# Optimization experiments

Measured on AMD Instinct MI355X. Metric: run time of the kernel, lower is better.

Reference implementation:

```python
import jax, jax.numpy as jnp
import numpy as np

B, S, H, NH = 2, 2048, 1024, 16
HD = H // NH  # 64


def rope_cos_sin(seq_len, dim, base=10000.0, dtype=jnp.float32):
    inv_freq = 1.0 / (base ** (jnp.arange(0, dim, 2, dtype=jnp.float32) / dim))
    t = jnp.arange(seq_len, dtype=jnp.float32)
    freqs = jnp.outer(t, inv_freq)              # [S, dim/2]
    emb = jnp.concatenate([freqs, freqs], -1)   # [S, dim]
    # broadcast shape [1, S, 1, dim]
    return jnp.cos(emb)[None, :, None, :].astype(dtype), jnp.sin(emb)[None, :, None, :].astype(dtype)


def rotate_half(x):
    x1, x2 = x[..., : x.shape[-1] // 2], x[..., x.shape[-1] // 2:]
    return jnp.concatenate([-x2, x1], axis=-1)


def setup_inputs() -> dict:
    key = jax.random.key(0)
    ks = jax.random.split(key, 5)
    sc = 1.0 / np.sqrt(H)
    x = jax.random.normal(ks[0], (B, S, H), jnp.float32)
    Wq = jax.random.normal(ks[1], (H, H), jnp.float32) * sc
    Wk = jax.random.normal(ks[2], (H, H), jnp.float32) * sc
    Wv = jax.random.normal(ks[3], (H, H), jnp.float32) * sc
    Wo = jax.random.normal(ks[4], (H, H), jnp.float32) * sc
    z = jnp.zeros((H,), jnp.float32)
    mask = jnp.tril(jnp.ones((S, S), bool))[None, None]  # causal [1,1,S,S]
    return {"x": x, "Wq": Wq, "bq": z, "Wk": Wk, "bk": z, "Wv": Wv, "bv": z,
            "Wo": Wo, "bo": z, "mask": mask}


def reference(x, Wq, bq, Wk, bk, Wv, bv, Wo, bo, mask):
    b, s, _ = x.shape
    q = (x @ Wq.T + bq).reshape(b, s, NH, HD)
    k = (x @ Wk.T + bk).reshape(b, s, NH, HD)
    v = (x @ Wv.T + bv).reshape(b, s, NH, HD)
    cos, sin = rope_cos_sin(s, HD, dtype=x.dtype)
    q = q * cos + rotate_half(q) * sin
    k = k * cos + rotate_half(k) * sin
    # [b, h, s, s] scores, explicit as in original
    scores = jnp.einsum("bqhd,bkhd->bhqk", q, k) / jnp.sqrt(jnp.asarray(HD, x.dtype))
    scores = jnp.where(mask, scores, jnp.asarray(-jnp.inf, x.dtype))
    attn = jax.nn.softmax(scores, axis=-1)
    out = jnp.einsum("bhqk,bkhd->bqhd", attn, v).reshape(b, s, H)
    return out @ Wo.T + bo
```

## Files before the change

### kernel.cpp

```cpp
#include <hip/hip_runtime.h>

typedef __bf16 bf16;
typedef __bf16 bf16x4 __attribute__((ext_vector_type(4)));
typedef __bf16 bf16x8 __attribute__((ext_vector_type(8)));
typedef float floatx4 __attribute__((ext_vector_type(4)));

#define MFMA16(a, b, c) __builtin_amdgcn_mfma_f32_16x16x32_bf16(a, b, c, 0, 0, 0)

__device__ __forceinline__ void load_lds16(const void* g, void* l) {
    __builtin_amdgcn_global_load_lds(
        (const __attribute__((address_space(1))) unsigned int*)g,
        (__attribute__((address_space(3))) unsigned int*)l, 16, 0, 0);
}

__device__ __forceinline__ bf16x8 scale8(bf16x8 a, float s) {
    bf16x8 o;
    #pragma unroll
    for (int i = 0; i < 8; i++) o[i] = (bf16)((float)a[i] * s);
    return o;
}

#define WAITV4_BAR()  do { asm volatile("s_waitcnt vmcnt(4)" ::: "memory"); \
                           __builtin_amdgcn_s_barrier();                    \
                           __builtin_amdgcn_sched_barrier(0); } while (0)
#define WAITV2_BAR()  do { asm volatile("s_waitcnt vmcnt(2)" ::: "memory"); \
                           __builtin_amdgcn_s_barrier();                    \
                           __builtin_amdgcn_sched_barrier(0); } while (0)
#define WAITV0_BAR()  do { asm volatile("s_waitcnt vmcnt(0)" ::: "memory"); \
                           __builtin_amdgcn_s_barrier();                    \
                           __builtin_amdgcn_sched_barrier(0); } while (0)
#define TRAIL_BAR()   do { __builtin_amdgcn_sched_barrier(0);               \
                           asm volatile("s_waitcnt lgkmcnt(0)" ::: "memory"); \
                           __builtin_amdgcn_s_barrier(); } while (0)

__global__ __launch_bounds__(256) void cvt_all_kernel(
    const float* __restrict__ x, const float* __restrict__ wq,
    const float* __restrict__ wk, const float* __restrict__ wv,
    const float* __restrict__ wo,
    bf16* __restrict__ xb, bf16* __restrict__ wqb, bf16* __restrict__ wkb,
    bf16* __restrict__ wvb, bf16* __restrict__ wob)
{
    int bid = blockIdx.x;
    const float* src; bf16* dst; int off;
    if (bid < 4096)      { src = x;  dst = xb;  off = bid; }
    else if (bid < 5120) { src = wq; dst = wqb; off = bid - 4096; }
    else if (bid < 6144) { src = wk; dst = wkb; off = bid - 5120; }
    else if (bid < 7168) { src = wv; dst = wvb; off = bid - 6144; }
    else                 { src = wo; dst = wob; off = bid - 7168; }
    int idx = (off * 256 + threadIdx.x) * 4;
    float4 v = *(const float4*)&src[idx];
    bf16x4 o;
    o[0] = (bf16)v.x; o[1] = (bf16)v.y; o[2] = (bf16)v.z; o[3] = (bf16)v.w;
    *(bf16x4*)&dst[idx] = o;
}

__global__ __launch_bounds__(256) void cvt_kernel(const float* __restrict__ x,
                                                  bf16* __restrict__ xb) {
    int idx = (blockIdx.x * 256 + threadIdx.x) * 4;
    float4 v = *(const float4*)&x[idx];
    bf16x4 o;
    o[0] = (bf16)v.x; o[1] = (bf16)v.y; o[2] = (bf16)v.z; o[3] = (bf16)v.w;
    *(bf16x4*)&xb[idx] = o;
}


#define PREP_STAGE()                                                          \
    int u0 = w * 128 + lane;                                                  \
    int u1 = u0 + 64;                                                         \
    int r0_ = u0 >> 2, c0_ = ((u0 & 3) ^ ((r0_ >> 1) & 3)) * 8;               \
    int r1_ = u1 >> 2, c1_ = ((u1 & 3) ^ ((r1_ >> 1) & 3)) * 8;               \
    int du0 = w * 1024;                                                       \
    int du1 = du0 + 512;

#define STAGE_PF(Asrc, Bsrc, arow, brow, sbuf, kk0)                           \
    do {                                                                      \
        load_lds16(&Asrc[(size_t)((arow) + r0_) * 1024 + (kk0) + c0_],        \
                   &As[sbuf][0][0] + du0);                                    \
        load_lds16(&Asrc[(size_t)((arow) + r1_) * 1024 + (kk0) + c1_],        \
                   &As[sbuf][0][0] + du1);                                    \
        load_lds16(&Bsrc[(size_t)((brow) + r0_) * 1024 + (kk0) + c0_],        \
                   &Bs[sbuf][0][0] + du0);                                    \
        load_lds16(&Bsrc[(size_t)((brow) + r1_) * 1024 + (kk0) + c1_],        \
                   &Bs[sbuf][0][0] + du1);                                    \
    } while (0)

#define GEMM_CORE(Asrc, Bsrc, arow, brow)                                     \
    PREP_STAGE()                                                              \
    STAGE_PF(Asrc, Bsrc, arow, brow, 0, 0);                                   \
    _Pragma("unroll 2")                                                       \
    for (int s = 0; s < 32; s++) {                                            \
        int sb = s & 1;                                                       \
        if (s + 1 < 32) {                                                     \
            STAGE_PF(Asrc, Bsrc, arow, brow, sb ^ 1, (s + 1) * 32);           \
            WAITV4_BAR();                                                     \
        } else {                                                              \
            WAITV0_BAR();                                                     \
        }                                                                     \
        bf16x8 af[4], bfr[4];                                                 \
        _Pragma("unroll")                                                     \
        for (int mt = 0; mt < 4; mt++) {                                      \
            int row = wm + mt * 16 + l15;                                     \
            af[mt] = *(const bf16x8*)&As[sb][row][(quad ^ ((row >> 1) & 3)) * 8]; \
        }                                                                     \
        _Pragma("unroll")                                                     \
        for (int nt = 0; nt < 4; nt++) {                                      \
            int row = wn + nt * 16 + l15;                                     \
            bfr[nt] = *(const bf16x8*)&Bs[sb][row][(quad ^ ((row >> 1) & 3)) * 8]; \
        }                                                                     \
        __builtin_amdgcn_s_setprio(1);                                        \
        _Pragma("unroll")                                                     \
        for (int mt = 0; mt < 4; mt++)                                        \
            _Pragma("unroll")                                                 \
            for (int nt = 0; nt < 4; nt++)                                    \
                acc[mt][nt] = MFMA16(af[mt], bfr[nt], acc[mt][nt]);           \
        __builtin_amdgcn_s_setprio(0);                                        \
        TRAIL_BAR();                                                          \
    }

__global__ __launch_bounds__(256) void gemm_qkv_fast(
    const bf16* __restrict__ xb,
    const bf16* __restrict__ Wq, const bf16* __restrict__ Wk,
    const bf16* __restrict__ Wv,
    const float* __restrict__ bq, const float* __restrict__ bk,
    const float* __restrict__ bv,
    bf16* __restrict__ q_ws, bf16* __restrict__ k_ws, bf16* __restrict__ vt_ws)
{
    int m0 = blockIdx.x * 128;
    int n0 = blockIdx.y * 128;
    int sec = n0 >> 10;
    int nw0 = n0 & 1023;
    const bf16* W     = (sec == 0) ? Wq : (sec == 1) ? Wk : Wv;
    const float* bias = (sec == 0) ? bq : (sec == 1) ? bk : bv;

    __shared__ bf16 As[2][128][32];
    __shared__ bf16 Bs[2][128][32];

    int tid = threadIdx.x;
    int lane = tid & 63, w = tid >> 6;
    int l15 = lane & 15, quad = lane >> 4;
    int wm = (w >> 1) * 64, wn = (w & 1) * 64;

    floatx4 acc[4][4];
    #pragma unroll
    for (int i = 0; i < 4; i++)
        #pragma unroll
        for (int j = 0; j < 4; j++) acc[i][j] = (floatx4){0.f, 0.f, 0.f, 0.f};

    GEMM_CORE(xb, W, m0, nw0)

    if (sec < 2) {
        bf16* outp = (sec == 0) ? q_ws : k_ws;
        float inv[2];
        inv[0] = __expf(-(float)l15 * (9.210340371976184f / 32.0f));
        inv[1] = __expf(-(float)(16 + l15) * (9.210340371976184f / 32.0f));
        #pragma unroll
        for (int mt = 0; mt < 4; mt++) {
            #pragma unroll
            for (int r = 0; r < 4; r++) {
                int m = m0 + wm + mt * 16 + quad * 4 + r;
                int bb = m >> 11, s = m & 2047;
                #pragma unroll
                for (int nt = 0; nt < 2; nt++) {
                    int nl1 = nw0 + wn + nt * 16 + l15;
                    int nl2 = nl1 + 32;
                    float x1 = acc[mt][nt][r] + bias[nl1];
                    float x2 = acc[mt][nt + 2][r] + bias[nl2];
                    float ang = (float)s * inv[nt];
                    float sn, cs;
                    __sincosf(ang, &sn, &cs);
                    int hh = nl1 >> 6, d = nl1 & 63;
                    size_t base = ((size_t)(bb * 16 + hh) * 2048 + s) * 64;
                    outp[base + d]      = (bf16)(x1 * cs - x2 * sn);
                    outp[base + d + 32] = (bf16)(x2 * cs + x1 * sn);
                }
            }
        }
    } else {
        #pragma unroll
        for (int mt = 0; mt < 4; mt++) {
            int mbase = m0 + wm + mt * 16 + quad * 4;
            int bb = mbase >> 11, s0 = mbase & 2047;
            #pragma unroll
            for (int nt = 0; nt < 4; nt++) {
                int nl = nw0 + wn + nt * 16 + l15;
                int hh = nl >> 6, d = nl & 63;
                bf16x4 pk;
                #pragma unroll
                for (int r = 0; r < 4; r++) pk[r] = (bf16)(acc[mt][nt][r] + bias[nl]);
                *(bf16x4*)&vt_ws[((size_t)(bb * 16 + hh) * 64 + d) * 2048 + s0] = pk;
            }
        }
    }
}

__global__ __launch_bounds__(256) void gemm_out_fast(
    const bf16* __restrict__ A, const bf16* __restrict__ W,
    const float* __restrict__ bias, float* __restrict__ out)
{
    int m0 = blockIdx.x * 128;
    int n0 = blockIdx.y * 128;

    __shared__ bf16 As[2][128][32];
    __shared__ bf16 Bs[2][128][32];

    int tid = threadIdx.x;
    int lane = tid & 63, w = tid >> 6;
    int l15 = lane & 15, quad = lane >> 4;
    int wm = (w >> 1) * 64, wn = (w & 1) * 64;

    floatx4 acc[4][4];
    #pragma unroll
    for (int i = 0; i < 4; i++)
        #pragma unroll
        for (int j = 0; j < 4; j++) acc[i][j] = (floatx4){0.f, 0.f, 0.f, 0.f};

    GEMM_CORE(A, W, m0, n0)

    #pragma unroll
    for (int mt = 0; mt < 4; mt++) {
        #pragma unroll
        for (int r = 0; r < 4; r++) {
            int m = m0 + wm + mt * 16 + quad * 4 + r;
            #pragma unroll
            for (int nt = 0; nt < 4; nt++) {
                int nl = n0 + wn + nt * 16 + l15;
                out[(size_t)m * 1024 + nl] = acc[mt][nt][r] + bias[nl];
            }
        }
    }
}

__global__ __launch_bounds__(256) void gemm_qkv_f32w(
    const bf16* __restrict__ xb,
    const float* __restrict__ Wq, const float* __restrict__ Wk,
    const float* __restrict__ Wv,
    const float* __restrict__ bq, const float* __restrict__ bk,
    const float* __restrict__ bv,
    bf16* __restrict__ q_ws, bf16* __restrict__ k_ws, bf16* __restrict__ vt_ws)
{
    int m0 = blockIdx.x * 128;
    int n0 = blockIdx.y * 128;
    int sec = n0 >> 10;
    int nw0 = n0 & 1023;
    const float* W    = (sec == 0) ? Wq : (sec == 1) ? Wk : Wv;
    const float* bias = (sec == 0) ? bq : (sec == 1) ? bk : bv;

    __shared__ bf16 As[128][72];
    __shared__ bf16 Bs[128][72];

    int tid = threadIdx.x;
    int lane = tid & 63, w = tid >> 6;
    int l15 = lane & 15, quad = lane >> 4;
    int wm = (w >> 1) * 64, wn = (w & 1) * 64;
    int sr = tid >> 1;
    int sk = (tid & 1) * 32;

    floatx4 acc[4][4];
    #pragma unroll
    for (int i = 0; i < 4; i++)
        #pragma unroll
        for (int j = 0; j < 4; j++) acc[i][j] = (floatx4){0.f, 0.f, 0.f, 0.f};

    for (int k0 = 0; k0 < 1024; k0 += 64) {
        __syncthreads();
        const bf16* ap = &xb[(size_t)(m0 + sr) * 1024 + k0 + sk];
        bf16x8 a0 = *(const bf16x8*)(ap);
        bf16x8 a1 = *(const bf16x8*)(ap + 8);
        bf16x8 a2 = *(const bf16x8*)(ap + 16);
        bf16x8 a3 = *(const bf16x8*)(ap + 24);
        const float* wp = &W[(size_t)(nw0 + sr) * 1024 + k0 + sk];
        bf16x8 bv_[4];
        #pragma unroll
        for (int c = 0; c < 4; c++) {
            float4 f0 = *(const float4*)(wp + c * 8);
            float4 f1 = *(const float4*)(wp + c * 8 + 4);
            bf16x8 t;
            t[0] = (bf16)f0.x; t[1] = (bf16)f0.y; t[2] = (bf16)f0.z; t[3] = (bf16)f0.w;
            t[4] = (bf16)f1.x; t[5] = (bf16)f1.y; t[6] = (bf16)f1.z; t[7] = (bf16)f1.w;
            bv_[c] = t;
        }
        *(bf16x8*)&As[sr][sk + 0]  = a0;
        *(bf16x8*)&As[sr][sk + 8]  = a1;
        *(bf16x8*)&As[sr][sk + 16] = a2;
        *(bf16x8*)&As[sr][sk + 24] = a3;
        #pragma unroll
        for (int c = 0; c < 4; c++) *(bf16x8*)&Bs[sr][sk + c * 8] = bv_[c];
        __syncthreads();
        #pragma unroll
        for (int kk = 0; kk < 64; kk += 32) {
            bf16x8 af[4], bfr[4];
            #pragma unroll
            for (int mt = 0; mt < 4; mt++)
                af[mt] = *(const bf16x8*)&As[wm + mt * 16 + l15][kk + quad * 8];
            #pragma unroll
            for (int nt = 0; nt < 4; nt++)
                bfr[nt] = *(const bf16x8*)&Bs[wn + nt * 16 + l15][kk + quad * 8];
            #pragma unroll
            for (int mt = 0; mt < 4; mt++)
                #pragma unroll
                for (int nt = 0; nt < 4; nt++)
                    acc[mt][nt] = MFMA16(af[mt], bfr[nt], acc[mt][nt]);
        }
    }

    if (sec < 2) {
        bf16* outp = (sec == 0) ? q_ws : k_ws;
        float inv[2];
        inv[0] = __expf(-(float)l15 * (9.210340371976184f / 32.0f));
        inv[1] = __expf(-(float)(16 + l15) * (9.210340371976184f / 32.0f));
        #pragma unroll
        for (int mt = 0; mt < 4; mt++) {
            #pragma unroll
            for (int r = 0; r < 4; r++) {
                int m = m0 + wm + mt * 16 + quad * 4 + r;
                int bb = m >> 11, s = m & 2047;
                #pragma unroll
                for (int nt = 0; nt < 2; nt++) {
                    int nl1 = nw0 + wn + nt * 16 + l15;
                    int nl2 = nl1 + 32;
                    float x1 = acc[mt][nt][r] + bias[nl1];
                    float x2 = acc[mt][nt + 2][r] + bias[nl2];
                    float ang = (float)s * inv[nt];
                    float sn, cs;
                    __sincosf(ang, &sn, &cs);
                    int hh = nl1 >> 6, d = nl1 & 63;
                    size_t base = ((size_t)(bb * 16 + hh) * 2048 + s) * 64;
                    outp[base + d]      = (bf16)(x1 * cs - x2 * sn);
                    outp[base + d + 32] = (bf16)(x2 * cs + x1 * sn);
                }
            }
        }
    } else {
        #pragma unroll
        for (int mt = 0; mt < 4; mt++) {
            int mbase = m0 + wm + mt * 16 + quad * 4;
            int bb = mbase >> 11, s0 = mbase & 2047;
            #pragma unroll
            for (int nt = 0; nt < 4; nt++) {
                int nl = nw0 + wn + nt * 16 + l15;
                int hh = nl >> 6, d = nl & 63;
                bf16x4 pk;
                #pragma unroll
                for (int r = 0; r < 4; r++) pk[r] = (bf16)(acc[mt][nt][r] + bias[nl]);
                *(bf16x4*)&vt_ws[((size_t)(bb * 16 + hh) * 64 + d) * 2048 + s0] = pk;
            }
        }
    }
}

__global__ __launch_bounds__(256) void gemm_out_f32w(
    const bf16* __restrict__ A, const float* __restrict__ W,
    const float* __restrict__ bias, float* __restrict__ out)
{
    int m0 = blockIdx.x * 128;
    int n0 = blockIdx.y * 128;

    __shared__ bf16 As[128][72];
    __shared__ bf16 Bs[128][72];

    int tid = threadIdx.x;
    int lane = tid & 63, w = tid >> 6;
    int l15 = lane & 15, quad = lane >> 4;
    int wm = (w >> 1) * 64, wn = (w & 1) * 64;
    int sr = tid >> 1;
    int sk = (tid & 1) * 32;

    floatx4 acc[4][4];
    #pragma unroll
    for (int i = 0; i < 4; i++)
        #pragma unroll
        for (int j = 0; j < 4; j++) acc[i][j] = (floatx4){0.f, 0.f, 0.f, 0.f};

    for (int k0 = 0; k0 < 1024; k0 += 64) {
        __syncthreads();
        const bf16* ap = &A[(size_t)(m0 + sr) * 1024 + k0 + sk];
        bf16x8 a0 = *(const bf16x8*)(ap);
        bf16x8 a1 = *(const bf16x8*)(ap + 8);
        bf16x8 a2 = *(const bf16x8*)(ap + 16);
        bf16x8 a3 = *(const bf16x8*)(ap + 24);
        const float* wp = &W[(size_t)(n0 + sr) * 1024 + k0 + sk];
        bf16x8 bv_[4];
        #pragma unroll
        for (int c = 0; c < 4; c++) {
            float4 f0 = *(const float4*)(wp + c * 8);
            float4 f1 = *(const float4*)(wp + c * 8 + 4);
            bf16x8 t;
            t[0] = (bf16)f0.x; t[1] = (bf16)f0.y; t[2] = (bf16)f0.z; t[3] = (bf16)f0.w;
            t[4] = (bf16)f1.x; t[5] = (bf16)f1.y; t[6] = (bf16)f1.z; t[7] = (bf16)f1.w;
            bv_[c] = t;
        }
        *(bf16x8*)&As[sr][sk + 0]  = a0;
        *(bf16x8*)&As[sr][sk + 8]  = a1;
        *(bf16x8*)&As[sr][sk + 16] = a2;
        *(bf16x8*)&As[sr][sk + 24] = a3;
        #pragma unroll
        for (int c = 0; c < 4; c++) *(bf16x8*)&Bs[sr][sk + c * 8] = bv_[c];
        __syncthreads();
        #pragma unroll
        for (int kk = 0; kk < 64; kk += 32) {
            bf16x8 af[4], bfr[4];
            #pragma unroll
            for (int mt = 0; mt < 4; mt++)
                af[mt] = *(const bf16x8*)&As[wm + mt * 16 + l15][kk + quad * 8];
            #pragma unroll
            for (int nt = 0; nt < 4; nt++)
                bfr[nt] = *(const bf16x8*)&Bs[wn + nt * 16 + l15][kk + quad * 8];
            #pragma unroll
            for (int mt = 0; mt < 4; mt++)
                #pragma unroll
                for (int nt = 0; nt < 4; nt++)
                    acc[mt][nt] = MFMA16(af[mt], bfr[nt], acc[mt][nt]);
        }
    }

    #pragma unroll
    for (int mt = 0; mt < 4; mt++) {
        #pragma unroll
        for (int r = 0; r < 4; r++) {
            int m = m0 + wm + mt * 16 + quad * 4 + r;
            #pragma unroll
            for (int nt = 0; nt < 4; nt++) {
                int nl = n0 + wn + nt * 16 + l15;
                out[(size_t)m * 1024 + nl] = acc[mt][nt][r] + bias[nl];
            }
        }
    }
}

__global__ __launch_bounds__(512, 4) void attn_kernel(
    const bf16* __restrict__ q_ws, const bf16* __restrict__ k_ws,
    const bf16* __restrict__ vt_ws, bf16* __restrict__ o_ws)
{
    __shared__ bf16 Ks[2][64][64];
    __shared__ bf16 Vt[2][64][64];
    __shared__ bf16 Ps[8][16][72];

    int tid = threadIdx.x;
    int w = tid >> 6, lane = tid & 63;
    int l15 = lane & 15, quad = lane >> 4;

    int bid = blockIdx.x;
    int g = bid & 31;
    int xx = bid >> 5;
    int qt = (xx < 8) ? xx : 23 - xx;
    if (g & 1) qt = 15 - qt;
    int bb = g >> 4, h = g & 15;
    const bf16* qp = q_ws + (size_t)g * 2048 * 64;
    const bf16* kp = k_ws + (size_t)g * 2048 * 64;
    const bf16* vp = vt_ws + (size_t)g * 64 * 2048;
    int qrow = qt * 128 + w * 16;

    int r = w * 8 + (lane >> 3);
    int c = (lane & 7) ^ (r & 7);
    int od = w * 512;

    const float SCL = 0.125f * 1.4426950408889634f;
    const float MFIX = 20.0f;

    bf16x8 qf0 = scale8(*(const bf16x8*)&qp[(size_t)(qrow + l15) * 64 + quad * 8], SCL);
    bf16x8 qf1 = scale8(*(const bf16x8*)&qp[(size_t)(qrow + l15) * 64 + 32 + quad * 8], SCL);

    float l_lane = 0.f;
    floatx4 acc[4];
    #pragma unroll
    for (int nt = 0; nt < 4; nt++) acc[nt] = (floatx4){0.f, 0.f, 0.f, 0.f};

    int nkt = 2 * qt + 2;

    load_lds16(&kp[(size_t)r * 64 + c * 8], &Ks[0][0][0] + od);
    load_lds16(&vp[(size_t)r * 2048 + c * 8], &Vt[0][0][0] + od);

    for (int kt = 0; kt < nkt; kt++) {
        int buf = kt & 1;
        if (kt + 1 < nkt) {
            int kn0 = (kt + 1) * 64;
            load_lds16(&kp[(size_t)(kn0 + r) * 64 + c * 8], &Ks[buf ^ 1][0][0] + od);
            load_lds16(&vp[(size_t)r * 2048 + kn0 + c * 8], &Vt[buf ^ 1][0][0] + od);
            WAITV2_BAR();
        } else {
            WAITV0_BAR();
        }

        int kt0 = kt * 64;

        floatx4 st[4];
        #pragma unroll
        for (int kb = 0; kb < 4; kb++) {
            int row = kb * 16 + l15;
            int rx = row & 7;
            bf16x8 a0 = *(const bf16x8*)&Ks[buf][row][(quad ^ rx) * 8];
            bf16x8 a1 = *(const bf16x8*)&Ks[buf][row][((quad + 4) ^ rx) * 8];
            floatx4 z = {-MFIX, -MFIX, -MFIX, -MFIX};
            __builtin_amdgcn_s_setprio(1);
            z = MFMA16(a0, qf0, z);
            z = MFMA16(a1, qf1, z);
            __builtin_amdgcn_s_setprio(0);
            st[kb] = z;
        }
        if (kt0 + 63 > qrow) {
            int q = qrow + l15;
            #pragma unroll
            for (int kb = 0; kb < 4; kb++)
                #pragma unroll
                for (int rr = 0; rr < 4; rr++) {
                    int key = kt0 + kb * 16 + quad * 4 + rr;
                    if (key > q) st[kb][rr] = -1e30f;
                }
        }

        #pragma unroll
        for (int kb = 0; kb < 4; kb++) {
            bf16x4 pk;
            #pragma unroll
            for (int rr = 0; rr < 4; rr++) {
                float pv = exp2f(st[kb][rr]);
                l_lane += pv;
                pk[rr] = (bf16)pv;
            }
            *(bf16x4*)&Ps[w][l15][kb * 16 + quad * 4] = pk;
        }

        bf16x8 pb0 = *(const bf16x8*)&Ps[w][l15][quad * 8];
        bf16x8 pb1 = *(const bf16x8*)&Ps[w][l15][32 + quad * 8];
        __builtin_amdgcn_s_setprio(1);
        #pragma unroll
        for (int nt = 0; nt < 4; nt++) {
            int row = nt * 16 + l15;
            int rx = row & 7;
            bf16x8 v0 = *(const bf16x8*)&Vt[buf][row][(quad ^ rx) * 8];
            bf16x8 v1 = *(const bf16x8*)&Vt[buf][row][((quad + 4) ^ rx) * 8];
            acc[nt] = MFMA16(v0, pb0, acc[nt]);
            acc[nt] = MFMA16(v1, pb1, acc[nt]);
        }
        __builtin_amdgcn_s_setprio(0);

        TRAIL_BAR();
    }

    l_lane += __shfl_xor(l_lane, 16, 64);
    l_lane += __shfl_xor(l_lane, 32, 64);
    float inv = 1.f / l_lane;
    int s = qrow + l15;
    #pragma unroll
    for (int nt = 0; nt < 4; nt++) {
        bf16x4 pk;
        #pragma unroll
        for (int rr = 0; rr < 4; rr++) pk[rr] = (bf16)(acc[nt][rr] * inv);
        *(bf16x4*)&o_ws[((size_t)(bb * 2048 + s)) * 1024 + h * 64 + nt * 16 + quad * 4] = pk;
    }
}

extern "C" void kernel_launch(void* const* d_in, const int* in_sizes, int n_in,
                              void* d_out, int out_size, void* d_ws, size_t ws_size,
                              hipStream_t stream) {
    const float* x  = (const float*)d_in[0];
    const float* Wq = (const float*)d_in[1];
    const float* bq = (const float*)d_in[2];
    const float* Wk = (const float*)d_in[3];
    const float* bk = (const float*)d_in[4];
    const float* Wv = (const float*)d_in[5];
    const float* bv = (const float*)d_in[6];
    const float* Wo = (const float*)d_in[7];
    const float* bo = (const float*)d_in[8];
    float* out = (float*)d_out;

    const size_t NELEM = (size_t)2 * 2048 * 1024;
    const size_t WELEM = (size_t)1024 * 1024;
    bf16* xb    = (bf16*)d_ws;
    bf16* q_ws  = xb + NELEM;
    bf16* k_ws  = q_ws + NELEM;
    bf16* vt_ws = k_ws + NELEM;
    bf16* o_ws  = xb;
    bf16* wqb   = vt_ws + NELEM;
    bf16* wkb   = wqb + WELEM;
    bf16* wvb   = wkb + WELEM;
    bf16* wob   = wvb + WELEM;

    bool fast = ws_size >= (size_t)40 * 1024 * 1024;

    if (fast) {
        cvt_all_kernel<<<8192, 256, 0, stream>>>(x, Wq, Wk, Wv, Wo,
                                                 xb, wqb, wkb, wvb, wob);
        gemm_qkv_fast<<<dim3(32, 24), 256, 0, stream>>>(
            xb, wqb, wkb, wvb, bq, bk, bv, q_ws, k_ws, vt_ws);
        attn_kernel<<<512, 512, 0, stream>>>(q_ws, k_ws, vt_ws, o_ws);
        gemm_out_fast<<<dim3(32, 8), 256, 0, stream>>>(o_ws, wob, bo, out);
    } else {
        cvt_kernel<<<4096, 256, 0, stream>>>(x, xb);
        gemm_qkv_f32w<<<dim3(32, 24), 256, 0, stream>>>(
            xb, Wq, Wk, Wv, bq, bk, bv, q_ws, k_ws, vt_ws);
        attn_kernel<<<512, 512, 0, stream>>>(q_ws, k_ws, vt_ws, o_ws);
        gemm_out_f32w<<<dim3(32, 8), 256, 0, stream>>>(o_ws, Wo, bo, out);
    }
}
```

Baseline: 202.6 us.

## Load K/V fragments directly from global into registers, drop LDS staging

Attention kernel no longer stages K and V tiles through shared memory with block barriers. Each wave now loads its K and V MFMA fragments straight from global memory into registers, double-buffering K across an unrolled pair of iterations. Each wave also stops at its own causal bound instead of the block-wide one, which skips masked tiles per wave. This removes the barriers and LDS traffic, but every wave re-reads K/V from global/L2 (8x redundant per block), uses more registers, and drops the occupancy hint.

```diff
diff --git a/kernel.cpp b/kernel.cpp
--- a/kernel.cpp
+++ b/kernel.cpp
@@ -21,9 +21,6 @@
 }
 
 #define WAITV4_BAR()  do { asm volatile("s_waitcnt vmcnt(4)" ::: "memory"); \
-                           __builtin_amdgcn_s_barrier();                    \
-                           __builtin_amdgcn_sched_barrier(0); } while (0)
-#define WAITV2_BAR()  do { asm volatile("s_waitcnt vmcnt(2)" ::: "memory"); \
                            __builtin_amdgcn_s_barrier();                    \
                            __builtin_amdgcn_sched_barrier(0); } while (0)
 #define WAITV0_BAR()  do { asm volatile("s_waitcnt vmcnt(0)" ::: "memory"); \
@@ -427,12 +424,71 @@
     }
 }
 
-__global__ __launch_bounds__(512, 4) void attn_kernel(
+#define ATTN_ITER(KT, KF, KN, DO_PRE)                                         \
+    do {                                                                      \
+        int kt0 = (KT) * 64;                                                  \
+        if (DO_PRE) {                                                         \
+            int kn0 = ((KT) + 1) * 64;                                        \
+            _Pragma("unroll")                                                 \
+            for (int kb = 0; kb < 4; kb++) {                                  \
+                const bf16* kr = &kp[(size_t)(kn0 + kb * 16 + l15) * 64];     \
+                KN[kb * 2]     = *(const bf16x8*)&kr[quad * 8];               \
+                KN[kb * 2 + 1] = *(const bf16x8*)&kr[32 + quad * 8];          \
+            }                                                                 \
+        }                                                                     \
+        floatx4 st[4];                                                        \
+        __builtin_amdgcn_s_setprio(1);                                        \
+        _Pragma("unroll")                                                     \
+        for (int kb = 0; kb < 4; kb++) {                                      \
+            floatx4 z = {-MFIX, -MFIX, -MFIX, -MFIX};                         \
+            z = MFMA16(KF[kb * 2], qf0, z);                                   \
+            z = MFMA16(KF[kb * 2 + 1], qf1, z);                               \
+            st[kb] = z;                                                       \
+        }                                                                     \
+        __builtin_amdgcn_s_setprio(0);                                        \
+        bf16x8 vf[8];                                                         \
+        _Pragma("unroll")                                                     \
+        for (int nt = 0; nt < 4; nt++) {                                      \
+            const bf16* vr = &vp[(size_t)(nt * 16 + l15) * 2048 + kt0];       \
+            vf[nt * 2]     = *(const bf16x8*)&vr[quad * 8];                   \
+            vf[nt * 2 + 1] = *(const bf16x8*)&vr[32 + quad * 8];              \
+        }                                                                     \
+        if (kt0 + 63 > qrow) {                                                \
+            int q = qrow + l15;                                               \
+            _Pragma("unroll")                                                 \
+            for (int kb = 0; kb < 4; kb++)                                    \
+                _Pragma("unroll")                                             \
+                for (int rr = 0; rr < 4; rr++) {                              \
+                    int key = kt0 + kb * 16 + quad * 4 + rr;                  \
+                    if (key > q) st[kb][rr] = -1e30f;                         \
+                }                                                             \
+        }                                                                     \
+        _Pragma("unroll")                                                     \
+        for (int kb = 0; kb < 4; kb++) {                                      \
+            bf16x4 pk;                                                        \
+            _Pragma("unroll")                                                 \
+            for (int rr = 0; rr < 4; rr++) {                                  \
+                float pv = exp2f(st[kb][rr]);                                 \
+                l_lane += pv;                                                 \
+                pk[rr] = (bf16)pv;                                            \
+            }                                                                 \
+            *(bf16x4*)&Ps[w][l15][kb * 16 + quad * 4] = pk;                   \
+        }                                                                     \
+        bf16x8 pb0 = *(const bf16x8*)&Ps[w][l15][quad * 8];                   \
+        bf16x8 pb1 = *(const bf16x8*)&Ps[w][l15][32 + quad * 8];              \
+        __builtin_amdgcn_s_setprio(1);                                        \
+        _Pragma("unroll")                                                     \
+        for (int nt = 0; nt < 4; nt++) {                                      \
+            acc[nt] = MFMA16(vf[nt * 2], pb0, acc[nt]);                       \
+            acc[nt] = MFMA16(vf[nt * 2 + 1], pb1, acc[nt]);                   \
+        }                                                                     \
+        __builtin_amdgcn_s_setprio(0);                                        \
+    } while (0)
+
+__global__ __launch_bounds__(512) void attn_kernel(
     const bf16* __restrict__ q_ws, const bf16* __restrict__ k_ws,
     const bf16* __restrict__ vt_ws, bf16* __restrict__ o_ws)
 {
-    __shared__ bf16 Ks[2][64][64];
-    __shared__ bf16 Vt[2][64][64];
     __shared__ bf16 Ps[8][16][72];
 
     int tid = threadIdx.x;
@@ -450,10 +506,6 @@
     const bf16* vp = vt_ws + (size_t)g * 64 * 2048;
     int qrow = qt * 128 + w * 16;
 
-    int r = w * 8 + (lane >> 3);
-    int c = (lane & 7) ^ (r & 7);
-    int od = w * 512;
-
     const float SCL = 0.125f * 1.4426950408889634f;
     const float MFIX = 20.0f;
 
@@ -465,77 +517,22 @@
     #pragma unroll
     for (int nt = 0; nt < 4; nt++) acc[nt] = (floatx4){0.f, 0.f, 0.f, 0.f};
 
-    int nkt = 2 * qt + 2;
-
-    load_lds16(&kp[(size_t)r * 64 + c * 8], &Ks[0][0][0] + od);
-    load_lds16(&vp[(size_t)r * 2048 + c * 8], &Vt[0][0][0] + od);
-
-    for (int kt = 0; kt < nkt; kt++) {
-        int buf = kt & 1;
-        if (kt + 1 < nkt) {
-            int kn0 = (kt + 1) * 64;
-            load_lds16(&kp[(size_t)(kn0 + r) * 64 + c * 8], &Ks[buf ^ 1][0][0] + od);
-            load_lds16(&vp[(size_t)r * 2048 + kn0 + c * 8], &Vt[buf ^ 1][0][0] + od);
-            WAITV2_BAR();
-        } else {
-            WAITV0_BAR();
-        }
-
-        int kt0 = kt * 64;
-
-        floatx4 st[4];
-        #pragma unroll
-        for (int kb = 0; kb < 4; kb++) {
-            int row = kb * 16 + l15;
-            int rx = row & 7;
-            bf16x8 a0 = *(const bf16x8*)&Ks[buf][row][(quad ^ rx) * 8];
-            bf16x8 a1 = *(const bf16x8*)&Ks[buf][row][((quad + 4) ^ rx) * 8];
-            floatx4 z = {-MFIX, -MFIX, -MFIX, -MFIX};
-            __builtin_amdgcn_s_setprio(1);
-            z = MFMA16(a0, qf0, z);
-            z = MFMA16(a1, qf1, z);
-            __builtin_amdgcn_s_setprio(0);
-            st[kb] = z;
-        }
-        if (kt0 + 63 > qrow) {
-            int q = qrow + l15;
-            #pragma unroll
-            for (int kb = 0; kb < 4; kb++)
-                #pragma unroll
-                for (int rr = 0; rr < 4; rr++) {
-                    int key = kt0 + kb * 16 + quad * 4 + rr;
-                    if (key > q) st[kb][rr] = -1e30f;
-                }
-        }
-
-        #pragma unroll
-        for (int kb = 0; kb < 4; kb++) {
-            bf16x4 pk;
-            #pragma unroll
-            for (int rr = 0; rr < 4; rr++) {
-                float pv = exp2f(st[kb][rr]);
-                l_lane += pv;
-                pk[rr] = (bf16)pv;
-            }
-            *(bf16x4*)&Ps[w][l15][kb * 16 + quad * 4] = pk;
-        }
-
-        bf16x8 pb0 = *(const bf16x8*)&Ps[w][l15][quad * 8];
-        bf16x8 pb1 = *(const bf16x8*)&Ps[w][l15][32 + quad * 8];
-        __builtin_amdgcn_s_setprio(1);
-        #pragma unroll
-        for (int nt = 0; nt < 4; nt++) {
-            int row = nt * 16 + l15;
-            int rx = row & 7;
-            bf16x8 v0 = *(const bf16x8*)&Vt[buf][row][(quad ^ rx) * 8];
-            bf16x8 v1 = *(const bf16x8*)&Vt[buf][row][((quad + 4) ^ rx) * 8];
-            acc[nt] = MFMA16(v0, pb0, acc[nt]);
-            acc[nt] = MFMA16(v1, pb1, acc[nt]);
-        }
-        __builtin_amdgcn_s_setprio(0);
-
-        TRAIL_BAR();
-    }
+    int nkt = ((qrow + 15) >> 6) + 1;
+
+    bf16x8 kfA[8], kfB[8];
+    #pragma unroll
+    for (int kb = 0; kb < 4; kb++) {
+        const bf16* kr = &kp[(size_t)(kb * 16 + l15) * 64];
+        kfA[kb * 2]     = *(const bf16x8*)&kr[quad * 8];
+        kfA[kb * 2 + 1] = *(const bf16x8*)&kr[32 + quad * 8];
+    }
+
+    int kt = 0;
+    for (; kt + 1 < nkt; kt += 2) {
+        ATTN_ITER(kt, kfA, kfB, true);
+        ATTN_ITER(kt + 1, kfB, kfA, (kt + 2 < nkt));
+    }
+    if (kt < nkt) ATTN_ITER(kt, kfA, kfB, false);
 
     l_lane += __shfl_xor(l_lane, 16, 64);
     l_lane += __shfl_xor(l_lane, 32, 64);
```

After: 299.1 us. 1.48x slower.

## Split attention KV tile across wave pairs with 32-row query tiles per wave

Applied to the files above, without the earlier changes.

Reorganizes the attention kernel so each wave handles 32 query rows and half of each 64-key tile, instead of 16 query rows over the full tile. Each loaded K/V fragment now feeds two query subtiles, halving LDS reads per MFMA. The two key-halves are combined at the end through shared memory, reusing the K/V buffers as scratch and adding a block-wide sync. This costs more registers for the accumulators and adds an epilogue reduction in which half of the waves sit idle.

```diff
diff --git a/kernel.cpp b/kernel.cpp
--- a/kernel.cpp
+++ b/kernel.cpp
@@ -431,13 +431,16 @@
     const bf16* __restrict__ q_ws, const bf16* __restrict__ k_ws,
     const bf16* __restrict__ vt_ws, bf16* __restrict__ o_ws)
 {
-    __shared__ bf16 Ks[2][64][64];
-    __shared__ bf16 Vt[2][64][64];
-    __shared__ bf16 Ps[8][16][72];
+    __shared__ __align__(16) char smem[32768];
+    bf16 (*Ks)[64][64] = (bf16(*)[64][64])smem;
+    bf16 (*Vt)[64][64] = (bf16(*)[64][64])(smem + 16384);
+    __shared__ bf16 Ps[4][32][72];
+    __shared__ float Lx[4][2][16];
 
     int tid = threadIdx.x;
     int w = tid >> 6, lane = tid & 63;
     int l15 = lane & 15, quad = lane >> 4;
+    int wq = w & 3, wk = w >> 2;
 
     int bid = blockIdx.x;
     int g = bid & 31;
@@ -448,7 +451,7 @@
     const bf16* qp = q_ws + (size_t)g * 2048 * 64;
     const bf16* kp = k_ws + (size_t)g * 2048 * 64;
     const bf16* vp = vt_ws + (size_t)g * 64 * 2048;
-    int qrow = qt * 128 + w * 16;
+    int qbase = qt * 128 + wq * 32;
 
     int r = w * 8 + (lane >> 3);
     int c = (lane & 7) ^ (r & 7);
@@ -457,13 +460,20 @@
     const float SCL = 0.125f * 1.4426950408889634f;
     const float MFIX = 20.0f;
 
-    bf16x8 qf0 = scale8(*(const bf16x8*)&qp[(size_t)(qrow + l15) * 64 + quad * 8], SCL);
-    bf16x8 qf1 = scale8(*(const bf16x8*)&qp[(size_t)(qrow + l15) * 64 + 32 + quad * 8], SCL);
-
-    float l_lane = 0.f;
-    floatx4 acc[4];
-    #pragma unroll
-    for (int nt = 0; nt < 4; nt++) acc[nt] = (floatx4){0.f, 0.f, 0.f, 0.f};
+    bf16x8 qf[2][2];
+    #pragma unroll
+    for (int qs = 0; qs < 2; qs++) {
+        const bf16* qr = &qp[(size_t)(qbase + qs * 16 + l15) * 64];
+        qf[qs][0] = scale8(*(const bf16x8*)&qr[quad * 8], SCL);
+        qf[qs][1] = scale8(*(const bf16x8*)&qr[32 + quad * 8], SCL);
+    }
+
+    float l_lane[2] = {0.f, 0.f};
+    floatx4 acc[4][2];
+    #pragma unroll
+    for (int db = 0; db < 4; db++)
+        #pragma unroll
+        for (int qs = 0; qs < 2; qs++) acc[db][qs] = (floatx4){0.f, 0.f, 0.f, 0.f};
 
     int nkt = 2 * qt + 2;
 
@@ -483,70 +493,103 @@
 
         int kt0 = kt * 64;
 
-        floatx4 st[4];
-        #pragma unroll
-        for (int kb = 0; kb < 4; kb++) {
-            int row = kb * 16 + l15;
+        floatx4 st[2][2];
+        #pragma unroll
+        for (int kb = 0; kb < 2; kb++) {
+            int row = wk * 32 + kb * 16 + l15;
             int rx = row & 7;
             bf16x8 a0 = *(const bf16x8*)&Ks[buf][row][(quad ^ rx) * 8];
             bf16x8 a1 = *(const bf16x8*)&Ks[buf][row][((quad + 4) ^ rx) * 8];
-            floatx4 z = {-MFIX, -MFIX, -MFIX, -MFIX};
             __builtin_amdgcn_s_setprio(1);
-            z = MFMA16(a0, qf0, z);
-            z = MFMA16(a1, qf1, z);
+            #pragma unroll
+            for (int qs = 0; qs < 2; qs++) {
+                floatx4 z = {-MFIX, -MFIX, -MFIX, -MFIX};
+                z = MFMA16(a0, qf[qs][0], z);
+                z = MFMA16(a1, qf[qs][1], z);
+                st[kb][qs] = z;
+            }
             __builtin_amdgcn_s_setprio(0);
-            st[kb] = z;
-        }
-        if (kt0 + 63 > qrow) {
-            int q = qrow + l15;
-            #pragma unroll
-            for (int kb = 0; kb < 4; kb++)
+        }
+
+        if (kt0 + wk * 32 + 31 > qbase) {
+            #pragma unroll
+            for (int kb = 0; kb < 2; kb++)
+                #pragma unroll
+                for (int qs = 0; qs < 2; qs++) {
+                    int q = qbase + qs * 16 + l15;
+                    #pragma unroll
+                    for (int rr = 0; rr < 4; rr++) {
+                        int key = kt0 + wk * 32 + kb * 16 + quad * 4 + rr;
+                        if (key > q) st[kb][qs][rr] = -1e30f;
+                    }
+                }
+        }
+
+        #pragma unroll
+        for (int kb = 0; kb < 2; kb++)
+            #pragma unroll
+            for (int qs = 0; qs < 2; qs++) {
+                bf16x4 pk;
                 #pragma unroll
                 for (int rr = 0; rr < 4; rr++) {
-                    int key = kt0 + kb * 16 + quad * 4 + rr;
-                    if (key > q) st[kb][rr] = -1e30f;
+                    float pv = exp2f(st[kb][qs][rr]);
+                    l_lane[qs] += pv;
+                    pk[rr] = (bf16)pv;
                 }
-        }
-
-        #pragma unroll
-        for (int kb = 0; kb < 4; kb++) {
-            bf16x4 pk;
-            #pragma unroll
-            for (int rr = 0; rr < 4; rr++) {
-                float pv = exp2f(st[kb][rr]);
-                l_lane += pv;
-                pk[rr] = (bf16)pv;
-            }
-            *(bf16x4*)&Ps[w][l15][kb * 16 + quad * 4] = pk;
-        }
-
-        bf16x8 pb0 = *(const bf16x8*)&Ps[w][l15][quad * 8];
-        bf16x8 pb1 = *(const bf16x8*)&Ps[w][l15][32 + quad * 8];
+                *(bf16x4*)&Ps[wq][qs * 16 + l15][wk * 32 + kb * 16 + quad * 4] = pk;
+            }
+
+        bf16x8 pb0 = *(const bf16x8*)&Ps[wq][l15][wk * 32 + quad * 8];
+        bf16x8 pb1 = *(const bf16x8*)&Ps[wq][16 + l15][wk * 32 + quad * 8];
         __builtin_amdgcn_s_setprio(1);
         #pragma unroll
-        for (int nt = 0; nt < 4; nt++) {
-            int row = nt * 16 + l15;
+        for (int db = 0; db < 4; db++) {
+            int row = db * 16 + l15;
             int rx = row & 7;
-            bf16x8 v0 = *(const bf16x8*)&Vt[buf][row][(quad ^ rx) * 8];
-            bf16x8 v1 = *(const bf16x8*)&Vt[buf][row][((quad + 4) ^ rx) * 8];
-            acc[nt] = MFMA16(v0, pb0, acc[nt]);
-            acc[nt] = MFMA16(v1, pb1, acc[nt]);
+            int ch = (wk * 4 + quad) ^ rx;
+            bf16x8 v = *(const bf16x8*)&Vt[buf][row][ch * 8];
+            acc[db][0] = MFMA16(v, pb0, acc[db][0]);
+            acc[db][1] = MFMA16(v, pb1, acc[db][1]);
         }
         __builtin_amdgcn_s_setprio(0);
 
         TRAIL_BAR();
     }
 
-    l_lane += __shfl_xor(l_lane, 16, 64);
-    l_lane += __shfl_xor(l_lane, 32, 64);
-    float inv = 1.f / l_lane;
-    int s = qrow + l15;
-    #pragma unroll
-    for (int nt = 0; nt < 4; nt++) {
-        bf16x4 pk;
-        #pragma unroll
-        for (int rr = 0; rr < 4; rr++) pk[rr] = (bf16)(acc[nt][rr] * inv);
-        *(bf16x4*)&o_ws[((size_t)(bb * 2048 + s)) * 1024 + h * 64 + nt * 16 + quad * 4] = pk;
+    #pragma unroll
+    for (int qs = 0; qs < 2; qs++) {
+        l_lane[qs] += __shfl_xor(l_lane[qs], 16, 64);
+        l_lane[qs] += __shfl_xor(l_lane[qs], 32, 64);
+    }
+
+    float* scr = (float*)smem;
+    if (wk == 1) {
+        #pragma unroll
+        for (int db = 0; db < 4; db++)
+            #pragma unroll
+            for (int qs = 0; qs < 2; qs++)
+                *(floatx4*)&scr[((wq * 8 + db * 2 + qs) * 64 + lane) * 4] = acc[db][qs];
+        Lx[wq][0][l15] = l_lane[0];
+        Lx[wq][1][l15] = l_lane[1];
+    }
+    __syncthreads();
+    if (wk == 0) {
+        float inv[2];
+        #pragma unroll
+        for (int qs = 0; qs < 2; qs++)
+            inv[qs] = 1.f / (l_lane[qs] + Lx[wq][qs][l15]);
+        #pragma unroll
+        for (int db = 0; db < 4; db++)
+            #pragma unroll
+            for (int qs = 0; qs < 2; qs++) {
+                floatx4 o = *(const floatx4*)&scr[((wq * 8 + db * 2 + qs) * 64 + lane) * 4];
+                bf16x4 pk;
+                #pragma unroll
+                for (int rr = 0; rr < 4; rr++)
+                    pk[rr] = (bf16)((acc[db][qs][rr] + o[rr]) * inv[qs]);
+                int s = qbase + qs * 16 + l15;
+                *(bf16x4*)&o_ws[((size_t)(bb * 2048 + s)) * 1024 + h * 64 + db * 16 + quad * 4] = pk;
+            }
     }
 }
 
```

New measurement: 197.9 us. -2.3%, faster.

## Halve attention query tile to 64 rows with 4-wave blocks and heaviest-first ordering

Applied to the files above, without the earlier changes.

The attention kernel now uses 256-thread blocks, each covering 64 query rows instead of 128, and launches 1024 blocks instead of 512. Each wave issues two K and two V async loads per tile to fill the 64x64 LDS tiles, so the wait count changes to vmcnt(4). Blocks are ordered so the causal tiles with the most work run first (qt = 31 - x), replacing the paired balanced mapping. The intent is finer-grained load balancing and more concurrent blocks per CU. In exchange, each K/V tile is reused by fewer query rows, which adds global and LDS traffic.

```diff
diff --git a/kernel.cpp b/kernel.cpp
--- a/kernel.cpp
+++ b/kernel.cpp
@@ -21,9 +21,6 @@
 }
 
 #define WAITV4_BAR()  do { asm volatile("s_waitcnt vmcnt(4)" ::: "memory"); \
-                           __builtin_amdgcn_s_barrier();                    \
-                           __builtin_amdgcn_sched_barrier(0); } while (0)
-#define WAITV2_BAR()  do { asm volatile("s_waitcnt vmcnt(2)" ::: "memory"); \
                            __builtin_amdgcn_s_barrier();                    \
                            __builtin_amdgcn_sched_barrier(0); } while (0)
 #define WAITV0_BAR()  do { asm volatile("s_waitcnt vmcnt(0)" ::: "memory"); \
@@ -427,13 +424,13 @@
     }
 }
 
-__global__ __launch_bounds__(512, 4) void attn_kernel(
+__global__ __launch_bounds__(256) void attn_kernel(
     const bf16* __restrict__ q_ws, const bf16* __restrict__ k_ws,
     const bf16* __restrict__ vt_ws, bf16* __restrict__ o_ws)
 {
     __shared__ bf16 Ks[2][64][64];
     __shared__ bf16 Vt[2][64][64];
-    __shared__ bf16 Ps[8][16][72];
+    __shared__ bf16 Ps[4][16][72];
 
     int tid = threadIdx.x;
     int w = tid >> 6, lane = tid & 63;
@@ -441,18 +438,20 @@
 
     int bid = blockIdx.x;
     int g = bid & 31;
-    int xx = bid >> 5;
-    int qt = (xx < 8) ? xx : 23 - xx;
-    if (g & 1) qt = 15 - qt;
+    int x = bid >> 5;
+    int qt = 31 - x;
     int bb = g >> 4, h = g & 15;
     const bf16* qp = q_ws + (size_t)g * 2048 * 64;
     const bf16* kp = k_ws + (size_t)g * 2048 * 64;
     const bf16* vp = vt_ws + (size_t)g * 64 * 2048;
-    int qrow = qt * 128 + w * 16;
-
-    int r = w * 8 + (lane >> 3);
-    int c = (lane & 7) ^ (r & 7);
-    int od = w * 512;
+    int qrow = qt * 64 + w * 16;
+
+    int g0 = (w * 2) * 64 + lane;
+    int g1 = g0 + 64;
+    int r0 = g0 >> 3, c0 = (g0 & 7) ^ (r0 & 7);
+    int r1 = g1 >> 3, c1 = (g1 & 7) ^ (r1 & 7);
+    int o0 = (w * 2) * 512;
+    int o1 = o0 + 512;
 
     const float SCL = 0.125f * 1.4426950408889634f;
     const float MFIX = 20.0f;
@@ -465,18 +464,22 @@
     #pragma unroll
     for (int nt = 0; nt < 4; nt++) acc[nt] = (floatx4){0.f, 0.f, 0.f, 0.f};
 
-    int nkt = 2 * qt + 2;
-
-    load_lds16(&kp[(size_t)r * 64 + c * 8], &Ks[0][0][0] + od);
-    load_lds16(&vp[(size_t)r * 2048 + c * 8], &Vt[0][0][0] + od);
+    int nkt = qt + 1;
+
+    load_lds16(&kp[(size_t)r0 * 64 + c0 * 8], &Ks[0][0][0] + o0);
+    load_lds16(&kp[(size_t)r1 * 64 + c1 * 8], &Ks[0][0][0] + o1);
+    load_lds16(&vp[(size_t)r0 * 2048 + c0 * 8], &Vt[0][0][0] + o0);
+    load_lds16(&vp[(size_t)r1 * 2048 + c1 * 8], &Vt[0][0][0] + o1);
 
     for (int kt = 0; kt < nkt; kt++) {
         int buf = kt & 1;
         if (kt + 1 < nkt) {
             int kn0 = (kt + 1) * 64;
-            load_lds16(&kp[(size_t)(kn0 + r) * 64 + c * 8], &Ks[buf ^ 1][0][0] + od);
-            load_lds16(&vp[(size_t)r * 2048 + kn0 + c * 8], &Vt[buf ^ 1][0][0] + od);
-            WAITV2_BAR();
+            load_lds16(&kp[(size_t)(kn0 + r0) * 64 + c0 * 8], &Ks[buf ^ 1][0][0] + o0);
+            load_lds16(&kp[(size_t)(kn0 + r1) * 64 + c1 * 8], &Ks[buf ^ 1][0][0] + o1);
+            load_lds16(&vp[(size_t)r0 * 2048 + kn0 + c0 * 8], &Vt[buf ^ 1][0][0] + o0);
+            load_lds16(&vp[(size_t)r1 * 2048 + kn0 + c1 * 8], &Vt[buf ^ 1][0][0] + o1);
+            WAITV4_BAR();
         } else {
             WAITV0_BAR();
         }
@@ -583,13 +586,13 @@
                                                  xb, wqb, wkb, wvb, wob);
         gemm_qkv_fast<<<dim3(32, 24), 256, 0, stream>>>(
             xb, wqb, wkb, wvb, bq, bk, bv, q_ws, k_ws, vt_ws);
-        attn_kernel<<<512, 512, 0, stream>>>(q_ws, k_ws, vt_ws, o_ws);
+        attn_kernel<<<1024, 256, 0, stream>>>(q_ws, k_ws, vt_ws, o_ws);
         gemm_out_fast<<<dim3(32, 8), 256, 0, stream>>>(o_ws, wob, bo, out);
     } else {
         cvt_kernel<<<4096, 256, 0, stream>>>(x, xb);
         gemm_qkv_f32w<<<dim3(32, 24), 256, 0, stream>>>(
             xb, Wq, Wk, Wv, bq, bk, bv, q_ws, k_ws, vt_ws);
-        attn_kernel<<<512, 512, 0, stream>>>(q_ws, k_ws, vt_ws, o_ws);
+        attn_kernel<<<1024, 256, 0, stream>>>(q_ws, k_ws, vt_ws, o_ws);
         gemm_out_f32w<<<dim3(32, 8), 256, 0, stream>>>(o_ws, Wo, bo, out);
     }
 }
```

Result: faster. 194.5 us (-4.0%).
